# Optimization experiments

Hardware: AMD Instinct MI355X
Metric: run time of the kernel (lower is better)

Reference implementation:

```python
import jax, jax.numpy as jnp
import numpy as np

B, T, D = 2, 2048, 2048
NH, NKV, HD = 16, 4, 128
EPS = 1e-6
SCALE = HD ** -0.5


def setup_inputs() -> dict:
    key = jax.random.key(0)
    ks = jax.random.split(key, 6)
    hidden = jax.random.normal(ks[0], (B, T, D), dtype=jnp.float32)
    # realistic RoPE tables: [B, T, HD], freqs repeated over both halves
    pos = jnp.arange(T, dtype=jnp.float32)
    inv_freq = 1.0 / (10000.0 ** (jnp.arange(0, HD, 2, dtype=jnp.float32) / HD))
    freqs = pos[:, None] * inv_freq[None, :]            # [T, HD/2]
    emb = jnp.concatenate([freqs, freqs], axis=-1)      # [T, HD]
    cos = jnp.broadcast_to(jnp.cos(emb)[None], (B, T, HD))
    sin = jnp.broadcast_to(jnp.sin(emb)[None], (B, T, HD))
    s = 0.02
    return {
        "hidden_BTD": hidden,
        "cos_BTK": cos,
        "sin_BTK": sin,
        "segment_ids_BT": jnp.zeros((B, T), dtype=jnp.int32),
        "position_ids_BT": jnp.broadcast_to(jnp.arange(T, dtype=jnp.int32)[None], (B, T)),
        "w_q": jax.random.normal(ks[1], (D, NH * HD * 2), dtype=jnp.float32) * s,
        "w_k": jax.random.normal(ks[2], (D, NKV * HD), dtype=jnp.float32) * s,
        "w_v": jax.random.normal(ks[3], (D, NKV * HD), dtype=jnp.float32) * s,
        "w_o": jax.random.normal(ks[4], (NH * HD, D), dtype=jnp.float32) * s,
        "q_norm_w": jnp.ones((HD,), dtype=jnp.float32),
        "k_norm_w": jnp.ones((HD,), dtype=jnp.float32),
    }


def _rms_norm(x, w):
    var = jnp.mean(jnp.square(x), axis=-1, keepdims=True)
    return x * jax.lax.rsqrt(var + EPS) * w


def _rotate_half(x):
    x1, x2 = jnp.split(x, 2, axis=-1)
    return jnp.concatenate([-x2, x1], axis=-1)


def _apply_rope(x, cos, sin):
    # x: [B,T,H,K]; cos/sin: [B,T,K] broadcast over heads
    c = cos[:, :, None, :]
    s = sin[:, :, None, :]
    return x * c + _rotate_half(x) * s


def reference(hidden_BTD, cos_BTK, sin_BTK, segment_ids_BT, position_ids_BT,
              w_q, w_k, w_v, w_o, q_norm_w, k_norm_w):
    Bn, Tn, _ = hidden_BTD.shape
    n_rep = NH // NKV
    # fused Q + gate projection, then split
    q_out = (hidden_BTD @ w_q).reshape(Bn, Tn, NH, HD * 2)
    q, gate = jnp.split(q_out, 2, axis=-1)                  # [B,T,H,K] each
    gate_BTD = gate.reshape(Bn, Tn, NH * HD)
    q = _rms_norm(q, q_norm_w)
    k = _rms_norm((hidden_BTD @ w_k).reshape(Bn, Tn, NKV, HD), k_norm_w)
    v = (hidden_BTD @ w_v).reshape(Bn, Tn, NKV, HD)
    q = _apply_rope(q, cos_BTK, sin_BTK)
    k = _apply_rope(k, cos_BTK, sin_BTK)
    # GQA: repeat kv heads
    k = jnp.repeat(k, n_rep, axis=2)                        # [B,T,H,K]
    v = jnp.repeat(v, n_rep, axis=2)
    scores = jnp.einsum('bqhk,bkhd->bhqd'.replace('d', 'K').replace('K', 'k') if False else 'bihk,bjhk->bhij', q, k) * SCALE
    causal = jnp.tril(jnp.ones((Tn, Tn), dtype=bool))
    scores = jnp.where(causal[None, None], scores, jnp.finfo(scores.dtype).min)
    probs = jax.nn.softmax(scores, axis=-1)
    attn = jnp.einsum('bhij,bjhk->bihk', probs, v)          # [B,T,H,K]
    attn_BTD = attn.reshape(Bn, Tn, NH * HD)
    attn_BTD = attn_BTD * jax.nn.sigmoid(gate_BTD)
    return attn_BTD @ w_o
```

## Files before the change

kernel.cpp:

```cpp
#include <hip/hip_runtime.h>
#include <hip/hip_bf16.h>

#define DEVI __device__ __forceinline__

typedef __attribute__((ext_vector_type(4))) float f32x4;
typedef __attribute__((ext_vector_type(8))) short s16x8;
typedef __attribute__((ext_vector_type(4))) short s16x4;

static constexpr int B_   = 2;
static constexpr int T_   = 2048;
static constexpr int D_   = 2048;
static constexpr int NH_  = 16;
static constexpr int NKV_ = 4;
static constexpr int HD_  = 128;
static constexpr int M_   = B_ * T_;
static constexpr int NQK  = NH_ * HD_ * 2;
static constexpr int NKC  = NKV_ * HD_;
static constexpr int NTOT = NQK + 2 * NKC;
static constexpr float SCALE_ = 0.08838834764831845f;

DEVI short f2bf(float f) {
    __hip_bfloat16 h = __float2bfloat16(f);
    return __builtin_bit_cast(short, h);
}
DEVI float bf2f(short s) {
    unsigned int u = ((unsigned int)(unsigned short)s) << 16;
    return __builtin_bit_cast(float, u);
}
DEVI void store_out(short* p, float v) { *p = f2bf(v); }
DEVI void store_out(float* p, float v) { *p = v; }

DEVI f32x4 mfma16(s16x8 a, s16x8 b, f32x4 c) {
    return __builtin_amdgcn_mfma_f32_16x16x32_bf16(a, b, c, 0, 0, 0);
}

DEVI void gload_lds16(const void* g, void* l) {
    __builtin_amdgcn_global_load_lds(
        (const __attribute__((address_space(1))) void*)g,
        (__attribute__((address_space(3))) void*)l,
        16, 0, 0);
}

__global__ void cast_f32_bf16(const float* __restrict__ in, short* __restrict__ out) {
    int i = (blockIdx.x * 256 + threadIdx.x) << 2;
    f32x4 v = *(const f32x4*)(in + i);
    s16x4 o;
#pragma unroll
    for (int j = 0; j < 4; ++j) o[j] = f2bf(v[j]);
    *(s16x4*)(out + i) = o;
}

__global__ void transpose_cast(const float* __restrict__ src, short* __restrict__ dst,
                               int R, int C) {
    __shared__ float tile[32][33];
    int c0 = blockIdx.x << 5, r0 = blockIdx.y << 5;
    int tx = threadIdx.x, ty = threadIdx.y;
#pragma unroll
    for (int i = 0; i < 32; i += 8)
        tile[ty + i][tx] = src[(long)(r0 + ty + i) * C + c0 + tx];
    __syncthreads();
#pragma unroll
    for (int i = 0; i < 32; i += 8)
        dst[(long)(c0 + ty + i) * R + r0 + tx] = f2bf(tile[tx][ty + i]);
}

template <typename OUT>
__global__ __launch_bounds__(256, 2) void gemm_bf16(
    const short* __restrict__ A, const short* __restrict__ Bt,
    OUT* __restrict__ C, int M, int N, int K) {
    __shared__ __align__(16) short Asm[2][128 * 32];
    __shared__ __align__(16) short Bsm[2][128 * 32];
    int tid = threadIdx.x;
    int nbx = N >> 7;
    int bx = blockIdx.x % nbx, by = blockIdx.x / nbx;
    int row0 = by << 7, col0 = bx << 7;
    int lane = tid & 63, wave = tid >> 6;
    int wr = (wave >> 1) << 6, wc = (wave & 1) << 6;
    int g = lane >> 4, rl = lane & 15;
    int srow = tid >> 2, scol = (tid & 3) << 3;
    const short* Ag = A + (long)(row0 + srow) * K + scol;
    const short* Bg = Bt + (long)(col0 + srow) * K + scol;

    f32x4 acc[4][4];
#pragma unroll
    for (int i = 0; i < 4; ++i)
#pragma unroll
        for (int j = 0; j < 4; ++j) acc[i][j] = f32x4{0.f, 0.f, 0.f, 0.f};

    auto stage = [&](int buf, int kt) {
        int ko = kt << 5;
        gload_lds16(Ag + ko,            &Asm[buf][tid * 8]);
        gload_lds16(Ag + (K << 6) + ko, &Asm[buf][(tid + 256) * 8]);
        gload_lds16(Bg + ko,            &Bsm[buf][tid * 8]);
        gload_lds16(Bg + (K << 6) + ko, &Bsm[buf][(tid + 256) * 8]);
    };

    int KT = K >> 5;
    stage(0, 0);
    for (int kt = 0; kt < KT; ++kt) {
        __syncthreads();
        int buf = kt & 1;
        if (kt + 1 < KT) stage(buf ^ 1, kt + 1);
        const short* As = &Asm[buf][0];
        const short* Bs = &Bsm[buf][0];
        s16x8 af[4], bfr[4];
#pragma unroll
        for (int i = 0; i < 4; ++i) {
            af[i]  = *(const s16x8*)(As + (wr + i * 16 + rl) * 32 + g * 8);
            bfr[i] = *(const s16x8*)(Bs + (wc + i * 16 + rl) * 32 + g * 8);
        }
#pragma unroll
        for (int i = 0; i < 4; ++i)
#pragma unroll
            for (int j = 0; j < 4; ++j)
                acc[i][j] = mfma16(af[i], bfr[j], acc[i][j]);
    }
#pragma unroll
    for (int i = 0; i < 4; ++i)
#pragma unroll
        for (int j = 0; j < 4; ++j)
#pragma unroll
            for (int r = 0; r < 4; ++r) {
                int row = row0 + wr + i * 16 + 4 * g + r;
                int col = col0 + wc + j * 16 + rl;
                store_out(&C[(long)row * N + col], acc[i][j][r]);
            }
}

__global__ void postproc(const short* __restrict__ qkv, const float* __restrict__ cosp,
                         const float* __restrict__ sinp, const float* __restrict__ qw,
                         const float* __restrict__ kw, short* __restrict__ Q,
                         short* __restrict__ K) {
    int task = blockIdx.x * 4 + (threadIdx.x >> 6);
    int lane = threadIdx.x & 63;
    int bt = task / 20, sub = task - bt * 20;
    int b = bt >> 11, t = bt & (T_ - 1);
    bool isq = sub < 16;
    int h = isq ? sub : sub - 16;
    const short* src = qkv + (long)bt * NTOT + (isq ? h * 256 : NQK + h * HD_);
    const float* w = isq ? qw : kw;
    float x0 = bf2f(src[lane]);
    float x1 = bf2f(src[lane + 64]);
    float ss = x0 * x0 + x1 * x1;
    ss += __shfl_xor(ss, 32); ss += __shfl_xor(ss, 16); ss += __shfl_xor(ss, 8);
    ss += __shfl_xor(ss, 4);  ss += __shfl_xor(ss, 2);  ss += __shfl_xor(ss, 1);
    float rn = rsqrtf(ss * (1.0f / 128.0f) + 1e-6f);
    x0 *= rn * w[lane];
    x1 *= rn * w[lane + 64];
    float c0 = cosp[bt * HD_ + lane], c1 = cosp[bt * HD_ + lane + 64];
    float s0 = sinp[bt * HD_ + lane], s1 = sinp[bt * HD_ + lane + 64];
    float y0 = x0 * c0 - x1 * s0;
    float y1 = x1 * c1 + x0 * s1;
    short* dst;
    if (isq) {
        y0 *= SCALE_; y1 *= SCALE_;
        dst = Q + ((long)(b * NH_ + h) * T_ + t) * HD_;
    } else {
        dst = K + ((long)(b * NKV_ + h) * T_ + t) * HD_;
    }
    dst[lane]      = f2bf(y0);
    dst[lane + 64] = f2bf(y1);
}

__global__ void transpose_v(const short* __restrict__ qkv, short* __restrict__ VT) {
    __shared__ short tile[32][33];
    int bh = blockIdx.z;
    int b = bh >> 2, h = bh & 3;
    int t0 = blockIdx.x << 5, d0 = blockIdx.y << 5;
    int tx = threadIdx.x, ty = threadIdx.y;
    const short* src = qkv + (long)b * T_ * NTOT + NQK + NKC + h * HD_;
#pragma unroll
    for (int i = 0; i < 32; i += 8)
        tile[ty + i][tx] = src[(long)(t0 + ty + i) * NTOT + d0 + tx];
    __syncthreads();
    short* dst = VT + ((long)(b * NKV_ + h) * HD_ + d0) * T_ + t0;
#pragma unroll
    for (int i = 0; i < 32; i += 8)
        dst[(long)(ty + i) * T_ + tx] = tile[tx][ty + i];
}

DEVI void softstep(f32x4& s0, f32x4& s1, float& m, float& l, f32x4 o[8],
                   s16x8& pa, int k0, int qb, int g, int rl) {
    if (k0 + 31 > qb) {
        int q = qb + rl;
#pragma unroll
        for (int r = 0; r < 4; ++r) {
            if (k0 + 4 * g + r > q)      s0[r] = -1e30f;
            if (k0 + 16 + 4 * g + r > q) s1[r] = -1e30f;
        }
    }
    float tm = fmaxf(fmaxf(fmaxf(s0[0], s0[1]), fmaxf(s0[2], s0[3])),
                     fmaxf(fmaxf(s1[0], s1[1]), fmaxf(s1[2], s1[3])));
    tm = fmaxf(tm, __shfl_xor(tm, 16));
    tm = fmaxf(tm, __shfl_xor(tm, 32));
    float mn = fmaxf(m, tm);
    float fr = __expf(m - mn);
    m = mn;
    float p[8];
#pragma unroll
    for (int r = 0; r < 4; ++r) {
        p[r]     = __expf(s0[r] - mn);
        p[4 + r] = __expf(s1[r] - mn);
    }
    float rs = ((p[0] + p[1]) + (p[2] + p[3])) + ((p[4] + p[5]) + (p[6] + p[7]));
    rs += __shfl_xor(rs, 16);
    rs += __shfl_xor(rs, 32);
    l = l * fr + rs;
    f32x4 fq;
#pragma unroll
    for (int r = 0; r < 4; ++r) fq[r] = __shfl(fr, 4 * g + r);
#pragma unroll
    for (int dt = 0; dt < 8; ++dt) o[dt] *= fq;
    s16x8 t;
#pragma unroll
    for (int i = 0; i < 8; ++i) t[i] = f2bf(p[i]);
    pa = t;
}

DEVI void epilogue(const f32x4 o[8], float l, int qb, int b, int h, int g, int rl,
                   const short* __restrict__ qkv, short* __restrict__ AG) {
    f32x4 linv;
#pragma unroll
    for (int r = 0; r < 4; ++r) linv[r] = 1.0f / __shfl(l, 4 * g + r);
#pragma unroll
    for (int r = 0; r < 4; ++r) {
        int qi = qb + 4 * g + r;
        long btr = (long)b * T_ + qi;
#pragma unroll
        for (int dt = 0; dt < 8; ++dt) {
            int d = dt * 16 + rl;
            float gate = bf2f(qkv[btr * NTOT + h * 256 + 128 + d]);
            float gv = 1.0f / (1.0f + __expf(-gate));
            AG[btr * (NH_ * HD_) + h * HD_ + d] = f2bf(o[dt][r] * linv[r] * gv);
        }
    }
}

__global__ __launch_bounds__(256) void fattn(
    const short* __restrict__ Q, const short* __restrict__ K,
    const short* __restrict__ VT, const short* __restrict__ qkv,
    short* __restrict__ AG) {
    int wave = threadIdx.x >> 6, lane = threadIdx.x & 63;
    int g = lane >> 4, rl = lane & 15;
    int grp = blockIdx.x & 7;
    int inner = blockIdx.x >> 3;
    int b = grp >> 2, kvh = grp & 3;
    int h = kvh * 4 + (inner >> 4);
    int j = ((inner & 15) << 2) + wave;
    int qbA = j << 4;
    int qbB = (127 - j) << 4;
    const short* Qp = Q + (long)(b * NH_ + h) * T_ * HD_;
    const short* Kp = K + (long)(b * NKV_ + kvh) * T_ * HD_;
    const short* Vp = VT + (long)(b * NKV_ + kvh) * HD_ * T_;

    s16x8 qfA[4], qfB[4];
#pragma unroll
    for (int c = 0; c < 4; ++c) {
        qfA[c] = *(const s16x8*)(Qp + (long)(qbA + rl) * HD_ + c * 32 + g * 8);
        qfB[c] = *(const s16x8*)(Qp + (long)(qbB + rl) * HD_ + c * 32 + g * 8);
    }

    f32x4 oA[8], oB[8];
#pragma unroll
    for (int dt = 0; dt < 8; ++dt) {
        oA[dt] = f32x4{0.f, 0.f, 0.f, 0.f};
        oB[dt] = f32x4{0.f, 0.f, 0.f, 0.f};
    }
    float mA = -1e30f, lA = 0.f, mB = -1e30f, lB = 0.f;

    int ntA = (qbA + 47) >> 5;
    int ntB = (qbB + 47) >> 5;

    for (int kt = 0; kt < ntB; ++kt) {
        int k0 = kt << 5;
        bool doA = kt < ntA;
        f32x4 sA0 = {0.f, 0.f, 0.f, 0.f}, sA1 = {0.f, 0.f, 0.f, 0.f};
        f32x4 sB0 = {0.f, 0.f, 0.f, 0.f}, sB1 = {0.f, 0.f, 0.f, 0.f};
#pragma unroll
        for (int c = 0; c < 4; ++c) {
            s16x8 kf0 = *(const s16x8*)(Kp + (long)(k0 + rl) * HD_ + c * 32 + g * 8);
            s16x8 kf1 = *(const s16x8*)(Kp + (long)(k0 + 16 + rl) * HD_ + c * 32 + g * 8);
            sB0 = mfma16(kf0, qfB[c], sB0);
            sB1 = mfma16(kf1, qfB[c], sB1);
            if (doA) {
                sA0 = mfma16(kf0, qfA[c], sA0);
                sA1 = mfma16(kf1, qfA[c], sA1);
            }
        }
        s16x8 paA, paB;
        softstep(sB0, sB1, mB, lB, oB, paB, k0, qbB, g, rl);
        if (doA) softstep(sA0, sA1, mA, lA, oA, paA, k0, qbA, g, rl);
#pragma unroll
        for (int dt = 0; dt < 8; ++dt) {
            const short* vp = Vp + (long)(dt * 16 + rl) * T_ + k0 + 4 * g;
            s16x4 v0 = *(const s16x4*)vp;
            s16x4 v1 = *(const s16x4*)(vp + 16);
            s16x8 vf = __builtin_shufflevector(v0, v1, 0, 1, 2, 3, 4, 5, 6, 7);
            oB[dt] = mfma16(paB, vf, oB[dt]);
            if (doA) oA[dt] = mfma16(paA, vf, oA[dt]);
        }
    }
    epilogue(oB, lB, qbB, b, h, g, rl, qkv, AG);
    epilogue(oA, lA, qbA, b, h, g, rl, qkv, AG);
}

extern "C" void kernel_launch(void* const* d_in, const int* in_sizes, int n_in,
                              void* d_out, int out_size, void* d_ws, size_t ws_size,
                              hipStream_t stream) {
    (void)in_sizes; (void)n_in; (void)out_size; (void)ws_size;
    const float* hidden = (const float*)d_in[0];
    const float* cosp   = (const float*)d_in[1];
    const float* sinp   = (const float*)d_in[2];
    const float* w_q    = (const float*)d_in[5];
    const float* w_k    = (const float*)d_in[6];
    const float* w_v    = (const float*)d_in[7];
    const float* w_o    = (const float*)d_in[8];
    const float* qnw    = (const float*)d_in[9];
    const float* knw    = (const float*)d_in[10];

    short* ws      = (short*)d_ws;
    short* hiddenb = ws;
    short* wqkvT   = hiddenb + (long)M_ * D_;
    short* woT     = wqkvT + (long)NTOT * D_;
    short* qkvb    = woT + (long)D_ * D_;
    short* Qb      = qkvb + (long)M_ * NTOT;
    short* Kb      = Qb + (long)B_ * NH_ * T_ * HD_;
    short* VTb     = Kb + (long)B_ * NKV_ * T_ * HD_;
    short* AGb     = VTb + (long)B_ * NKV_ * T_ * HD_;
    float* out     = (float*)d_out;

    dim3 tblk(32, 8);
    cast_f32_bf16<<<(M_ * D_) / 1024, 256, 0, stream>>>(hidden, hiddenb);
    transpose_cast<<<dim3(NQK / 32, D_ / 32), tblk, 0, stream>>>(w_q, wqkvT, D_, NQK);
    transpose_cast<<<dim3(NKC / 32, D_ / 32), tblk, 0, stream>>>(w_k, wqkvT + (long)NQK * D_, D_, NKC);
    transpose_cast<<<dim3(NKC / 32, D_ / 32), tblk, 0, stream>>>(w_v, wqkvT + (long)(NQK + NKC) * D_, D_, NKC);
    transpose_cast<<<dim3(D_ / 32, D_ / 32), tblk, 0, stream>>>(w_o, woT, D_, D_);

    gemm_bf16<short><<<(M_ / 128) * (NTOT / 128), 256, 0, stream>>>(
        hiddenb, wqkvT, qkvb, M_, NTOT, D_);

    postproc<<<(M_ * 20) / 4, 256, 0, stream>>>(qkvb, cosp, sinp, qnw, knw, Qb, Kb);
    transpose_v<<<dim3(T_ / 32, HD_ / 32, B_ * NKV_), tblk, 0, stream>>>(qkvb, VTb);

    fattn<<<512, 256, 0, stream>>>(Qb, Kb, VTb, qkvb, AGb);

    gemm_bf16<float><<<(M_ / 128) * (D_ / 128), 256, 0, stream>>>(
        AGb, woT, out, M_, D_, D_);
}
```

Before: 675.7 us.

## Give each attention wave one query tile and double the grid

Each wave of the flash-attention kernel now handles a single 16-row query block instead of a paired short/long causal pair. The four waves of a block take mirrored indices so the block as a whole still has balanced causal work. The grid doubles to 1024 blocks. This cuts register pressure (one accumulator set) and raises parallelism, at the cost of less K/V reuse per wave and some imbalance between waves inside a block.

```diff
diff --git a/kernel.cpp b/kernel.cpp
--- a/kernel.cpp
+++ b/kernel.cpp
@@ -245,63 +245,49 @@
     int grp = blockIdx.x & 7;
     int inner = blockIdx.x >> 3;
     int b = grp >> 2, kvh = grp & 3;
-    int h = kvh * 4 + (inner >> 4);
-    int j = ((inner & 15) << 2) + wave;
-    int qbA = j << 4;
-    int qbB = (127 - j) << 4;
+    int h = kvh * 4 + (inner >> 5);
+    int bi = inner & 31;
+    int j = (wave == 0) ? bi : (wave == 1) ? 63 - bi
+          : (wave == 2) ? 64 + bi : 127 - bi;
+    int qb = j << 4;
     const short* Qp = Q + (long)(b * NH_ + h) * T_ * HD_;
     const short* Kp = K + (long)(b * NKV_ + kvh) * T_ * HD_;
     const short* Vp = VT + (long)(b * NKV_ + kvh) * HD_ * T_;
 
-    s16x8 qfA[4], qfB[4];
-#pragma unroll
-    for (int c = 0; c < 4; ++c) {
-        qfA[c] = *(const s16x8*)(Qp + (long)(qbA + rl) * HD_ + c * 32 + g * 8);
-        qfB[c] = *(const s16x8*)(Qp + (long)(qbB + rl) * HD_ + c * 32 + g * 8);
-    }
-
-    f32x4 oA[8], oB[8];
-#pragma unroll
-    for (int dt = 0; dt < 8; ++dt) {
-        oA[dt] = f32x4{0.f, 0.f, 0.f, 0.f};
-        oB[dt] = f32x4{0.f, 0.f, 0.f, 0.f};
-    }
-    float mA = -1e30f, lA = 0.f, mB = -1e30f, lB = 0.f;
-
-    int ntA = (qbA + 47) >> 5;
-    int ntB = (qbB + 47) >> 5;
-
-    for (int kt = 0; kt < ntB; ++kt) {
+    s16x8 qf[4];
+#pragma unroll
+    for (int c = 0; c < 4; ++c)
+        qf[c] = *(const s16x8*)(Qp + (long)(qb + rl) * HD_ + c * 32 + g * 8);
+
+    f32x4 o[8];
+#pragma unroll
+    for (int dt = 0; dt < 8; ++dt) o[dt] = f32x4{0.f, 0.f, 0.f, 0.f};
+    float m = -1e30f, l = 0.f;
+
+    int nt = (qb + 47) >> 5;
+
+    for (int kt = 0; kt < nt; ++kt) {
         int k0 = kt << 5;
-        bool doA = kt < ntA;
-        f32x4 sA0 = {0.f, 0.f, 0.f, 0.f}, sA1 = {0.f, 0.f, 0.f, 0.f};
-        f32x4 sB0 = {0.f, 0.f, 0.f, 0.f}, sB1 = {0.f, 0.f, 0.f, 0.f};
+        f32x4 s0 = {0.f, 0.f, 0.f, 0.f}, s1 = {0.f, 0.f, 0.f, 0.f};
 #pragma unroll
         for (int c = 0; c < 4; ++c) {
             s16x8 kf0 = *(const s16x8*)(Kp + (long)(k0 + rl) * HD_ + c * 32 + g * 8);
             s16x8 kf1 = *(const s16x8*)(Kp + (long)(k0 + 16 + rl) * HD_ + c * 32 + g * 8);
-            sB0 = mfma16(kf0, qfB[c], sB0);
-            sB1 = mfma16(kf1, qfB[c], sB1);
-            if (doA) {
-                sA0 = mfma16(kf0, qfA[c], sA0);
-                sA1 = mfma16(kf1, qfA[c], sA1);
-            }
-        }
-        s16x8 paA, paB;
-        softstep(sB0, sB1, mB, lB, oB, paB, k0, qbB, g, rl);
-        if (doA) softstep(sA0, sA1, mA, lA, oA, paA, k0, qbA, g, rl);
+            s0 = mfma16(kf0, qf[c], s0);
+            s1 = mfma16(kf1, qf[c], s1);
+        }
+        s16x8 pa;
+        softstep(s0, s1, m, l, o, pa, k0, qb, g, rl);
 #pragma unroll
         for (int dt = 0; dt < 8; ++dt) {
             const short* vp = Vp + (long)(dt * 16 + rl) * T_ + k0 + 4 * g;
             s16x4 v0 = *(const s16x4*)vp;
             s16x4 v1 = *(const s16x4*)(vp + 16);
             s16x8 vf = __builtin_shufflevector(v0, v1, 0, 1, 2, 3, 4, 5, 6, 7);
-            oB[dt] = mfma16(paB, vf, oB[dt]);
-            if (doA) oA[dt] = mfma16(paA, vf, oA[dt]);
-        }
-    }
-    epilogue(oB, lB, qbB, b, h, g, rl, qkv, AG);
-    epilogue(oA, lA, qbA, b, h, g, rl, qkv, AG);
+            o[dt] = mfma16(pa, vf, o[dt]);
+        }
+    }
+    epilogue(o, l, qb, b, h, g, rl, qkv, AG);
 }
 
 extern "C" void kernel_launch(void* const* d_in, const int* in_sizes, int n_in,
@@ -342,7 +328,7 @@
     postproc<<<(M_ * 20) / 4, 256, 0, stream>>>(qkvb, cosp, sinp, qnw, knw, Qb, Kb);
     transpose_v<<<dim3(T_ / 32, HD_ / 32, B_ * NKV_), tblk, 0, stream>>>(qkvb, VTb);
 
-    fattn<<<512, 256, 0, stream>>>(Qb, Kb, VTb, qkvb, AGb);
+    fattn<<<1024, 256, 0, stream>>>(Qb, Kb, VTb, qkvb, AGb);
 
     gemm_bf16<float><<<(M_ / 128) * (D_ / 128), 256, 0, stream>>>(
         AGb, woT, out, M_, D_, D_);
```

After: 691.9 us. 2.4% more time.
